# Optimization experiments

Measured on AMD Instinct MI355X. Metric: run time of the kernel, lower is better.

The kernel has to match this reference:

```python
import jax, jax.numpy as jnp
import numpy as np

TARGET_MAIN_CONTRIBUTION = 0.6
CONTRIB_LOSS_COEF = 0.01
TOP_K = 2
NEG_INF = -1e9


def _gat(x, adj, W1, a1s, a1d, W2, a2s, a2d):
    """Dense 2-layer GAT (pyGAT style): multi-head concat + ELU, then one output head.
    x: [B,S,Fin], adj: [B,S,S], W1: [H,Fin,Fh], a1s/a1d: [H,Fh], W2: [H*Fh,Fout], a2s/a2d: [Fout]."""
    mask = adj > 0  # [B,S,S]
    h = jnp.einsum('bsf,hfo->bhso', x, W1)                      # [B,H,S,Fh]
    es = jnp.einsum('bhso,ho->bhs', h, a1s)
    ed = jnp.einsum('bhso,ho->bhs', h, a1d)
    e = jax.nn.leaky_relu(es[:, :, :, None] + ed[:, :, None, :], 0.2)  # [B,H,S,S]
    att = jax.nn.softmax(jnp.where(mask[:, None], e, NEG_INF), axis=-1)
    h1 = jax.nn.elu(jnp.einsum('bhst,bhto->bhso', att, h))      # [B,H,S,Fh]
    B, H, S, Fh = h1.shape
    h1 = h1.transpose(0, 2, 1, 3).reshape(B, S, H * Fh)         # concat heads
    h2 = h1 @ W2                                                # [B,S,Fout]
    e2 = jax.nn.leaky_relu((h2 @ a2s)[:, :, None] + (h2 @ a2d)[:, None, :], 0.2)
    att2 = jax.nn.softmax(jnp.where(mask, e2, NEG_INF), axis=-1)
    return jnp.einsum('bst,bto->bso', att2, h2)


def setup_inputs() -> dict:
    B, S, D, H, Hd, E = 4, 1024, 256, 6, 64, 3
    key = jax.random.key(0)
    ks = jax.random.split(key, 20)
    feature = jax.random.normal(ks[0], (B, S, D), dtype=jnp.float32)
    # sparse-ish binary adjacency with self-loops
    adj = (jax.random.uniform(ks[1], (B, S, S)) < 0.05).astype(jnp.float32)
    adj = jnp.maximum(adj, jnp.eye(S, dtype=jnp.float32)[None])
    p = lambda k, shape: jax.random.normal(k, shape, dtype=jnp.float32) * 0.1
    return {
        'feature': feature, 'adj': adj,
        'main_W1': p(ks[2], (H, D, Hd)), 'main_a1s': p(ks[3], (H, Hd)), 'main_a1d': p(ks[4], (H, Hd)),
        'main_W2': p(ks[5], (H * Hd, D)), 'main_a2s': p(ks[6], (D,)), 'main_a2d': p(ks[7], (D,)),
        'dep_W1': p(ks[8], (E, H, D, Hd)), 'dep_a1s': p(ks[9], (E, H, Hd)), 'dep_a1d': p(ks[10], (E, H, Hd)),
        'dep_W2': p(ks[11], (E, H * Hd, D)), 'dep_a2s': p(ks[12], (E, D)), 'dep_a2d': p(ks[13], (E, D)),
        'router_W': p(ks[14], (D, E)),
        'blend_W': p(ks[15], (D, D)), 'blend_b': jnp.zeros((D,), dtype=jnp.float32),
        'doc_num': 4, 'sect_num': 32,
    }


def reference(feature, adj, main_W1, main_a1s, main_a1d, main_W2, main_a2s, main_a2d,
              dep_W1, dep_a1s, dep_a1d, dep_W2, dep_a2s, dep_a2d,
              router_W, blend_W, blend_b, doc_num, sect_num):
    B, S, D = feature.shape
    E = router_W.shape[1]
    # main expert on full graph
    main_output = _gat(feature, adj, main_W1, main_a1s, main_a1d, main_W2, main_a2s, main_a2d)
    # per-expert adjacency views (zero out columns by node type)
    col = jnp.arange(S)
    sent_cols = (col < S - sect_num - doc_num).astype(adj.dtype)
    sect_cols = ((col >= S - sect_num - doc_num) & (col < S - doc_num)).astype(adj.dtype)
    doc_cols = (col >= S - doc_num).astype(adj.dtype)
    adj_stack = jnp.stack([adj * sent_cols, adj * sect_cols, adj * doc_cols])  # [E,B,S,S]
    # fixed top-k router
    x_flat = feature.reshape(-1, D)
    gate_probs = jax.nn.softmax(x_flat @ router_W, axis=-1)      # [B*S,E]
    _, top_idx = jax.lax.top_k(gate_probs, TOP_K)                # [B*S,k]
    routing_mask = jax.nn.one_hot(top_idx, E, dtype=feature.dtype).sum(axis=-2)  # [B*S,E] binary
    routing_mask = routing_mask.reshape(B, S, E)
    mask_e = routing_mask.transpose(2, 0, 1)[..., None]          # [E,B,S,1]
    # deputy experts: masked input, masked output, accumulate
    x_e = feature[None] * mask_e                                 # [E,B,S,D]
    dep_out = jax.vmap(_gat)(x_e, adj_stack, dep_W1, dep_a1s, dep_a1d, dep_W2, dep_a2s, dep_a2d)
    deputy_output = (dep_out * mask_e).sum(axis=0)               # [B,S,D]
    # blend gate
    blend_weight = jax.nn.sigmoid(feature @ blend_W + blend_b)
    final_output = blend_weight * main_output + (1.0 - blend_weight) * deputy_output
    main_contribution = blend_weight.mean()
    contribution_loss = jnp.abs(main_contribution - TARGET_MAIN_CONTRIBUTION) * CONTRIB_LOSS_COEF
    return final_output, contribution_loss, main_contribution
```

## Files before the change

### kernel.cpp

```cpp
#include <hip/hip_runtime.h>
#include <math.h>

#define B 4
#define S 1024
#define D 256
#define H 6
#define HD 64
#define NE 3
#define HHD 384
#define ROWS (B*S)
#define MAXN 128

typedef __attribute__((ext_vector_type(8))) short bf8_t;
typedef __attribute__((ext_vector_type(4))) float f32x4;

__device__ __forceinline__ float leaky(float x){ return x > 0.f ? x : 0.2f*x; }

__device__ __forceinline__ unsigned short f2bf(float f){
    union { float f; unsigned int u; } v; v.f = f;
    unsigned int u = v.u;
    return (unsigned short)((u + 0x7FFFu + ((u >> 16) & 1u)) >> 16);
}
__device__ __forceinline__ float bf2f(unsigned short h){
    union { unsigned int u; float f; } v; v.u = ((unsigned int)h) << 16;
    return v.f;
}
__device__ __forceinline__ float blo(unsigned int u){
    union { unsigned int u; float f; } v; v.u = u << 16; return v.f;
}
__device__ __forceinline__ float bhi(unsigned int u){
    union { unsigned int u; float f; } v; v.u = u & 0xffff0000u; return v.f;
}
__device__ __forceinline__ float i2f(int t){
    union { int i; float f; } v; v.i = t; return v.f;
}
__device__ __forceinline__ int f2i(float f){
    union { float f; int i; } v; v.f = f; return v.i;
}

#define PB_CONV   1024
#define PB_NBR    1024
#define PB_W1     1536
#define PB_W2     1536
#define PB_BW      256
#define PB_ZERO    177
#define PB_ROUTER 1024
#define PB_TOTAL  (PB_CONV + PB_NBR + PB_W1 + PB_W2 + PB_BW + PB_ZERO + PB_ROUTER)
#define NZERO     45088

__global__ __launch_bounds__(256) void prep_misc_kernel(
        const float* __restrict__ feature, const float* __restrict__ adj,
        const float* __restrict__ main_W1, const float* __restrict__ dep_W1,
        const float* __restrict__ main_W2, const float* __restrict__ dep_W2,
        const float* __restrict__ blend_W, const float* __restrict__ router_W,
        const int* __restrict__ doc_p, const int* __restrict__ sect_p,
        unsigned short* __restrict__ featbf, short* __restrict__ nbr,
        int4* __restrict__ nbc, unsigned short* __restrict__ w1nk,
        unsigned short* __restrict__ w2nk, unsigned short* __restrict__ bwt,
        float* __restrict__ zbase, float* __restrict__ rmask)
{
    int blk = blockIdx.x, tid = threadIdx.x;
    if (blk < PB_CONV){
        int idx = blk*256 + tid;
        float4 v = ((const float4*)feature)[idx];
        ushort4 o;
        o.x = f2bf(v.x); o.y = f2bf(v.y); o.z = f2bf(v.z); o.w = f2bf(v.w);
        ((ushort4*)featbf)[idx] = o;
        return;
    }
    blk -= PB_CONV;
    if (blk < PB_NBR){
        int wave = tid >> 6, lane = tid & 63;
        int row = blk*4 + wave;
        int b1 = S - *sect_p - *doc_p;
        int b2 = S - *doc_p;
        const float* ar = adj + (size_t)row*S + lane*16;
        float a[16];
        #pragma unroll
        for (int q = 0; q < 4; q++){
            float4 v = ((const float4*)ar)[q];
            a[q*4+0] = v.x; a[q*4+1] = v.y; a[q*4+2] = v.z; a[q*4+3] = v.w;
        }
        int t0 = lane*16;
        int k = 0, c1 = 0, c2 = 0;
        #pragma unroll
        for (int i = 0; i < 16; i++){
            if (a[i] > 0.f){
                k++;
                int t = t0 + i;
                if (t < b1) c1++;
                if (t < b2) c2++;
            }
        }
        int inc = k;
        #pragma unroll
        for (int d = 1; d < 64; d <<= 1){
            int u = __shfl_up(inc, d);
            if (lane >= d) inc += u;
        }
        int off = inc - k;
        int total = __shfl(inc, 63);
        int o = row*MAXN + off;
        #pragma unroll
        for (int i = 0; i < 16; i++){
            if (a[i] > 0.f) nbr[o++] = (short)(t0 + i);
        }
        for (int d = 32; d; d >>= 1){
            c1 += __shfl_down(c1, d);
            c2 += __shfl_down(c2, d);
        }
        if (lane == 0) nbc[row] = make_int4(total, c1, c2, 0);
        return;
    }
    blk -= PB_NBR;
    if (blk < PB_W1){
        int e = blk / 384;
        int idx = (blk - e*384)*256 + tid;
        const float* src = (e == 0) ? main_W1 : dep_W1 + (size_t)(e-1)*H*D*HD;
        int n = idx >> 8, k = idx & 255;
        int h = n >> 6, o = n & 63;
        w1nk[(size_t)e*HHD*D + idx] = f2bf(src[(h*D + k)*HD + o]);
        return;
    }
    blk -= PB_W1;
    if (blk < PB_W2){
        int g = blk*256 + tid;
        int e = g / (D*HHD);
        int rem = g - e*(D*HHD);
        int n = rem / HHD, k = rem - n*HHD;
        const float* src = (e == 0) ? main_W2 : dep_W2 + (size_t)(e-1)*HHD*D;
        w2nk[g] = f2bf(src[k*D + n]);
        return;
    }
    blk -= PB_W2;
    if (blk < PB_BW){
        int col = blk, k = tid;
        bwt[col*D + k] = f2bf(blend_W[k*D + col]);
        return;
    }
    blk -= PB_BW;
    if (blk < PB_ZERO){
        int idx = blk*256 + tid;
        if (idx < NZERO) zbase[idx] = 0.f;
        return;
    }
    blk -= PB_ZERO;
    {
        int wave = tid >> 6, lane = tid & 63;
        int row = blk*4 + wave;
        float4 xv = ((const float4*)(feature + (size_t)row*D))[lane];
        int f = lane*4;
        float xa[4] = {xv.x, xv.y, xv.z, xv.w};
        float p0 = 0.f, p1 = 0.f, p2 = 0.f;
        #pragma unroll
        for (int j = 0; j < 4; j++){
            p0 += xa[j]*router_W[(f+j)*NE + 0];
            p1 += xa[j]*router_W[(f+j)*NE + 1];
            p2 += xa[j]*router_W[(f+j)*NE + 2];
        }
        for (int off = 32; off; off >>= 1){
            p0 += __shfl_down(p0, off);
            p1 += __shfl_down(p1, off);
            p2 += __shfl_down(p2, off);
        }
        if (lane == 0){
            float p[3] = {p0, p1, p2};
            int ex = 0;
            for (int e = 1; e < NE; e++) if (p[e] <= p[ex]) ex = e;
            for (int e = 0; e < NE; e++) rmask[e*ROWS + row] = (e == ex) ? 0.f : 1.f;
        }
    }
}

__global__ __launch_bounds__(256, 4) void gemm1_kernel(const unsigned short* __restrict__ w1nk,
                                                    const unsigned short* __restrict__ featbf,
                                                    const float* __restrict__ rmask,
                                                    const float* __restrict__ main_a1s,
                                                    const float* __restrict__ main_a1d,
                                                    const float* __restrict__ dep_a1s,
                                                    const float* __restrict__ dep_a1d,
                                                    const unsigned short* __restrict__ bwt,
                                                    const float* __restrict__ bb,
                                                    unsigned short* __restrict__ htn4,
                                                    float* __restrict__ es8,
                                                    float* __restrict__ ed8,
                                                    float* __restrict__ meanV1p,
                                                    float* __restrict__ gatebuf,
                                                    float* __restrict__ sumBuf){
    __shared__ float ep[2][2][64][17];
    int tid = threadIdx.x, wave = tid >> 6, lane = tid & 63;
    int quad = lane >> 4, l16 = lane & 15;
    int e = blockIdx.z;
    int n0 = blockIdx.y*64;
    f32x4 z4 = {0.f,0.f,0.f,0.f};
    bf8_t bz = {0,0,0,0,0,0,0,0};

    if (e == 4){
        if (blockIdx.x >= 2) return;
        int m0 = blockIdx.x*128;
        const unsigned short* arow0 = bwt + (size_t)(m0 + wave*16 + l16)*D + quad*8;
        const unsigned short* arow1 = arow0 + (size_t)64*D;
        const unsigned short* brow[4];
        #pragma unroll
        for (int j = 0; j < 4; j++)
            brow[j] = featbf + (size_t)(n0 + j*16 + l16)*D + quad*8;
        f32x4 acc[8] = {z4, z4, z4, z4, z4, z4, z4, z4};
        bf8_t a0F = *(const bf8_t*)(arow0);
        bf8_t a1F = *(const bf8_t*)(arow1);
        bf8_t bF[4];
        #pragma unroll
        for (int j = 0; j < 4; j++) bF[j] = *(const bf8_t*)(brow[j]);
        #pragma unroll
        for (int it = 0; it < D/32; it++){
            bf8_t a0C = a0F, a1C = a1F;
            bf8_t bC[4] = {bF[0], bF[1], bF[2], bF[3]};
            if (it + 1 < D/32){
                int kn = (it + 1)*32;
                a0F = *(const bf8_t*)(arow0 + kn);
                a1F = *(const bf8_t*)(arow1 + kn);
                #pragma unroll
                for (int j = 0; j < 4; j++) bF[j] = *(const bf8_t*)(brow[j] + kn);
            }
            #pragma unroll
            for (int j = 0; j < 4; j++){
                acc[j]   = __builtin_amdgcn_mfma_f32_16x16x32_bf16(a0C, bC[j], acc[j],   0, 0, 0);
                acc[4+j] = __builtin_amdgcn_mfma_f32_16x16x32_bf16(a1C, bC[j], acc[4+j], 0, 0, 0);
            }
        }
        int mbase0 = m0 + wave*16 + quad*4;
        int mbase1 = mbase0 + 64;
        float bias0[4], bias1[4];
        #pragma unroll
        for (int r = 0; r < 4; r++){ bias0[r] = bb[mbase0 + r]; bias1[r] = bb[mbase1 + r]; }
        float lsum = 0.f;
        #pragma unroll
        for (int j = 0; j < 4; j++){
            int rown = n0 + j*16 + l16;
            f32x4 st0, st1;
            #pragma unroll
            for (int r = 0; r < 4; r++){
                float g0 = 1.f/(1.f + __expf(-(acc[j][r] + bias0[r])));
                float g1 = 1.f/(1.f + __expf(-(acc[4+j][r] + bias1[r])));
                lsum += g0 + g1;
                st0[r] = g0; st1[r] = g1;
            }
            *(f32x4*)(gatebuf + (size_t)rown*D + mbase0) = st0;
            *(f32x4*)(gatebuf + (size_t)rown*D + mbase1) = st1;
        }
        float* redp = &ep[0][0][0][0];
        redp[tid] = lsum;
        __syncthreads();
        for (int sft = 128; sft; sft >>= 1){
            if (tid < sft) redp[tid] += redp[tid + sft];
            __syncthreads();
        }
        if (tid == 0) atomicAdd(sumBuf, redp[0]);
        return;
    }

    int p = blockIdx.x;
    int m0 = p*128;
    const unsigned short* arow0 = w1nk + (size_t)e*HHD*D + (size_t)(m0 + wave*16 + l16)*D + quad*8;
    const unsigned short* arow1 = arow0 + (size_t)64*D;
    const unsigned short* brow[4];
    bool zr[4];
    #pragma unroll
    for (int j = 0; j < 4; j++){
        int n = n0 + j*16 + l16;
        brow[j] = featbf + (size_t)n*D + quad*8;
        zr[j] = (e > 0) ? (rmask[(size_t)(e-1)*ROWS + n] == 0.f) : false;
    }
    f32x4 acc[8] = {z4, z4, z4, z4, z4, z4, z4, z4};
    bf8_t a0F = *(const bf8_t*)(arow0);
    bf8_t a1F = *(const bf8_t*)(arow1);
    bf8_t bF[4];
    #pragma unroll
    for (int j = 0; j < 4; j++) bF[j] = zr[j] ? bz : *(const bf8_t*)(brow[j]);
    #pragma unroll
    for (int it = 0; it < D/32; it++){
        bf8_t a0C = a0F, a1C = a1F;
        bf8_t bC[4] = {bF[0], bF[1], bF[2], bF[3]};
        if (it + 1 < D/32){
            int kn = (it + 1)*32;
            a0F = *(const bf8_t*)(arow0 + kn);
            a1F = *(const bf8_t*)(arow1 + kn);
            #pragma unroll
            for (int j = 0; j < 4; j++) bF[j] = zr[j] ? bz : *(const bf8_t*)(brow[j] + kn);
        }
        #pragma unroll
        for (int j = 0; j < 4; j++){
            acc[j]   = __builtin_amdgcn_mfma_f32_16x16x32_bf16(a0C, bC[j], acc[j],   0, 0, 0);
            acc[4+j] = __builtin_amdgcn_mfma_f32_16x16x32_bf16(a1C, bC[j], acc[4+j], 0, 0, 0);
        }
    }
    int b = n0 >> 10;
    int mbase0 = m0 + wave*16 + quad*4;
    int mbase1 = mbase0 + 64;
    int obase = wave*16 + quad*4;
    int h0 = p*2, h1 = p*2 + 1;
    #pragma unroll
    for (int j = 0; j < 4; j++){
        int row = n0 + j*16 + l16;
        ushort4 o0, o1;
        o0.x = f2bf(acc[j][0]);   o0.y = f2bf(acc[j][1]);
        o0.z = f2bf(acc[j][2]);   o0.w = f2bf(acc[j][3]);
        o1.x = f2bf(acc[4+j][0]); o1.y = f2bf(acc[4+j][1]);
        o1.z = f2bf(acc[4+j][2]); o1.w = f2bf(acc[4+j][3]);
        *(ushort4*)(htn4 + ((size_t)e*ROWS + row)*HHD + mbase0) = o0;
        *(ushort4*)(htn4 + ((size_t)e*ROWS + row)*HHD + mbase1) = o1;
    }
    const float* a1sp = (e == 0) ? main_a1s : dep_a1s + (size_t)(e-1)*H*HD;
    const float* a1dp = (e == 0) ? main_a1d : dep_a1d + (size_t)(e-1)*H*HD;
    float s0v[4], d0v[4], s1v[4], d1v[4];
    #pragma unroll
    for (int r = 0; r < 4; r++){
        s0v[r] = a1sp[mbase0 + r]; d0v[r] = a1dp[mbase0 + r];
        s1v[r] = a1sp[mbase1 + r]; d1v[r] = a1dp[mbase1 + r];
    }
    #pragma unroll
    for (int j = 0; j < 4; j++){
        float ps0 = 0.f, pd0 = 0.f, ps1 = 0.f, pd1 = 0.f;
        #pragma unroll
        for (int r = 0; r < 4; r++){
            ps0 += acc[j][r]*s0v[r];   pd0 += acc[j][r]*d0v[r];
            ps1 += acc[4+j][r]*s1v[r]; pd1 += acc[4+j][r]*d1v[r];
        }
        ep[0][0][j*16 + l16][wave*4 + quad] = ps0;
        ep[0][1][j*16 + l16][wave*4 + quad] = pd0;
        ep[1][0][j*16 + l16][wave*4 + quad] = ps1;
        ep[1][1][j*16 + l16][wave*4 + quad] = pd1;
    }
    float* mvb = meanV1p + ((size_t)e*B + b)*512;
    #pragma unroll
    for (int r = 0; r < 4; r++){
        float cm0 = acc[0][r] + acc[1][r] + acc[2][r] + acc[3][r];
        float cm1 = acc[4][r] + acc[5][r] + acc[6][r] + acc[7][r];
        for (int off = 8; off; off >>= 1){
            cm0 += __shfl_down(cm0, off, 16);
            cm1 += __shfl_down(cm1, off, 16);
        }
        if (l16 == 0){
            atomicAdd(mvb + (obase + r)*8 + h0, cm0*(1.f/(float)S));
            atomicAdd(mvb + (obase + r)*8 + h1, cm1*(1.f/(float)S));
        }
    }
    __syncthreads();
    {
        int hh = tid >> 7, arr = (tid >> 6) & 1, sl = tid & 63;
        float sum = 0.f;
        #pragma unroll
        for (int i = 0; i < 16; i++) sum += ep[hh][arr][sl][i];
        int n = n0 + sl;
        float* dst = arr ? ed8 : es8;
        dst[(((size_t)e*B + (n >> 10))*S + (n & 1023))*8 + (p*2 + hh)] = sum;
    }
}

__global__ __launch_bounds__(256) void attn1_gather_kernel(const unsigned short* __restrict__ htn4,
                                                           const float* __restrict__ es8,
                                                           const float* __restrict__ ed8,
                                                           const short* __restrict__ nbr,
                                                           const int4* __restrict__ nbc,
                                                           const float* __restrict__ meanV1p,
                                                           unsigned short* __restrict__ h1c4){
    __shared__ float wrec[4][MAXN][8];
    int wave = threadIdx.x >> 6, lane = threadIdx.x & 63;
    int s = blockIdx.x*4 + wave;
    int e = blockIdx.y >> 2, b = blockIdx.y & 3;
    int row = b*S + s;
    int4 c = nbc[row];
    int lo = 0, hi = c.x;
    if (e == 1) hi = c.y;
    else if (e == 2){ lo = c.y; hi = c.z; }
    else if (e == 3){ lo = c.z; }
    int nn = hi - lo;
    const float* esp = es8 + (((size_t)e*B + b)*S + s)*8;
    f32x4 es_lo = *(const f32x4*)esp;
    f32x4 es_hi = *(const f32x4*)(esp + 4);
    float esv[6] = {es_lo[0], es_lo[1], es_lo[2], es_lo[3], es_hi[0], es_hi[1]};
    const float* edb = ed8 + (((size_t)e*B + b)*S)*8;
    const short* nl = nbr + (size_t)row*MAXN;
    float w0[6] = {0,0,0,0,0,0}, w1[6] = {0,0,0,0,0,0};
    int t0 = 0, t1 = 0;
    if (lane < nn){
        t0 = nl[lo + lane];
        const float* ep = edb + (size_t)t0*8;
        f32x4 d0 = *(const f32x4*)ep;
        f32x4 d1 = *(const f32x4*)(ep + 4);
        float edv[6] = {d0[0], d0[1], d0[2], d0[3], d1[0], d1[1]};
        #pragma unroll
        for (int h = 0; h < 6; h++) w0[h] = __expf(leaky(esv[h] + edv[h]));
    }
    if (64 + lane < nn){
        t1 = nl[lo + 64 + lane];
        const float* ep = edb + (size_t)t1*8;
        f32x4 d0 = *(const f32x4*)ep;
        f32x4 d1 = *(const f32x4*)(ep + 4);
        float edv[6] = {d0[0], d0[1], d0[2], d0[3], d1[0], d1[1]};
        #pragma unroll
        for (int h = 0; h < 6; h++) w1[h] = __expf(leaky(esv[h] + edv[h]));
    }
    float den[6];
    #pragma unroll
    for (int h = 0; h < 6; h++){
        float d = w0[h] + w1[h];
        for (int o2 = 32; o2; o2 >>= 1) d += __shfl_down(d, o2);
        den[h] = __shfl(d, 0);
    }
    if (lane < nn){
        f32x4 r0 = {w0[0], w0[1], w0[2], w0[3]};
        f32x4 r1 = {w0[4], w0[5], i2f(t0), 0.f};
        *(f32x4*)&wrec[wave][lane][0] = r0;
        *(f32x4*)&wrec[wave][lane][4] = r1;
    }
    if (64 + lane < nn){
        f32x4 r0 = {w1[0], w1[1], w1[2], w1[3]};
        f32x4 r1 = {w1[4], w1[5], i2f(t1), 0.f};
        *(f32x4*)&wrec[wave][64 + lane][0] = r0;
        *(f32x4*)&wrec[wave][64 + lane][4] = r1;
    }
    const unsigned short* Vb = htn4 + ((size_t)e*ROWS + b*S)*HHD + lane;
    float acc[6] = {0,0,0,0,0,0};
    #pragma unroll 4
    for (int j = 0; j < nn; j++){
        f32x4 r0 = *(const f32x4*)&wrec[wave][j][0];
        f32x4 r1 = *(const f32x4*)&wrec[wave][j][4];
        int t = f2i(r1[2]);
        const unsigned short* vp = Vb + (size_t)t*HHD;
        float v0 = bf2f(vp[0]);
        float v1 = bf2f(vp[64]);
        float v2 = bf2f(vp[128]);
        float v3 = bf2f(vp[192]);
        float v4 = bf2f(vp[256]);
        float v5 = bf2f(vp[320]);
        acc[0] += r0[0]*v0; acc[1] += r0[1]*v1;
        acc[2] += r0[2]*v2; acc[3] += r0[3]*v3;
        acc[4] += r1[0]*v4; acc[5] += r1[1]*v5;
    }
    unsigned short* outp = h1c4 + ((size_t)e*ROWS + row)*HHD;
    const float* mv = meanV1p + ((size_t)e*B + b)*512 + lane*8;
    #pragma unroll
    for (int h = 0; h < 6; h++){
        float v = (nn > 0) ? acc[h]/den[h] : mv[h];
        v = v > 0.f ? v : __expf(v) - 1.f;
        outp[h*64 + lane] = f2bf(v);
    }
}

__global__ __launch_bounds__(256, 4) void gemm2_kernel(const unsigned short* __restrict__ w2nk,
                                                    const unsigned short* __restrict__ h1c4,
                                                    const float* __restrict__ main_a2s,
                                                    const float* __restrict__ main_a2d,
                                                    const float* __restrict__ dep_a2s,
                                                    const float* __restrict__ dep_a2d,
                                                    unsigned short* __restrict__ h2n4,
                                                    float* __restrict__ f2s4,
                                                    float* __restrict__ f2d4,
                                                    float* __restrict__ meanV2){
    __shared__ float ep[2][2][64][17];
    int tid = threadIdx.x, wave = tid >> 6, lane = tid & 63;
    int quad = lane >> 4, l16 = lane & 15;
    int e = blockIdx.z;
    int m0 = blockIdx.x*128;
    int n0 = blockIdx.y*64;
    f32x4 z4 = {0.f,0.f,0.f,0.f};
    const unsigned short* arow0 = w2nk + (size_t)e*D*HHD + (size_t)(m0 + wave*16 + l16)*HHD + quad*8;
    const unsigned short* arow1 = arow0 + (size_t)64*HHD;
    const unsigned short* brow[4];
    #pragma unroll
    for (int j = 0; j < 4; j++)
        brow[j] = h1c4 + (size_t)e*ROWS*HHD + (size_t)(n0 + j*16 + l16)*HHD + quad*8;
    f32x4 acc[8] = {z4, z4, z4, z4, z4, z4, z4, z4};
    bf8_t a0F = *(const bf8_t*)(arow0);
    bf8_t a1F = *(const bf8_t*)(arow1);
    bf8_t bF[4];
    #pragma unroll
    for (int j = 0; j < 4; j++) bF[j] = *(const bf8_t*)(brow[j]);
    #pragma unroll
    for (int it = 0; it < HHD/32; it++){
        bf8_t a0C = a0F, a1C = a1F;
        bf8_t bC[4] = {bF[0], bF[1], bF[2], bF[3]};
        if (it + 1 < HHD/32){
            int kn = (it + 1)*32;
            a0F = *(const bf8_t*)(arow0 + kn);
            a1F = *(const bf8_t*)(arow1 + kn);
            #pragma unroll
            for (int j = 0; j < 4; j++) bF[j] = *(const bf8_t*)(brow[j] + kn);
        }
        #pragma unroll
        for (int j = 0; j < 4; j++){
            acc[j]   = __builtin_amdgcn_mfma_f32_16x16x32_bf16(a0C, bC[j], acc[j],   0, 0, 0);
            acc[4+j] = __builtin_amdgcn_mfma_f32_16x16x32_bf16(a1C, bC[j], acc[4+j], 0, 0, 0);
        }
    }
    int b = n0 >> 10;
    int mbase0 = m0 + wave*16 + quad*4;
    int mbase1 = mbase0 + 64;
    #pragma unroll
    for (int j = 0; j < 4; j++){
        int row = n0 + j*16 + l16;
        ushort4 o0, o1;
        o0.x = f2bf(acc[j][0]);   o0.y = f2bf(acc[j][1]);
        o0.z = f2bf(acc[j][2]);   o0.w = f2bf(acc[j][3]);
        o1.x = f2bf(acc[4+j][0]); o1.y = f2bf(acc[4+j][1]);
        o1.z = f2bf(acc[4+j][2]); o1.w = f2bf(acc[4+j][3]);
        *(ushort4*)(h2n4 + ((size_t)e*ROWS + row)*D + mbase0) = o0;
        *(ushort4*)(h2n4 + ((size_t)e*ROWS + row)*D + mbase1) = o1;
    }
    const float* a2sp = (e == 0) ? main_a2s : dep_a2s + (size_t)(e-1)*D;
    const float* a2dp = (e == 0) ? main_a2d : dep_a2d + (size_t)(e-1)*D;
    float s0v[4], d0v[4], s1v[4], d1v[4];
    #pragma unroll
    for (int r = 0; r < 4; r++){
        s0v[r] = a2sp[mbase0 + r]; d0v[r] = a2dp[mbase0 + r];
        s1v[r] = a2sp[mbase1 + r]; d1v[r] = a2dp[mbase1 + r];
    }
    #pragma unroll
    for (int j = 0; j < 4; j++){
        float ps0 = 0.f, pd0 = 0.f, ps1 = 0.f, pd1 = 0.f;
        #pragma unroll
        for (int r = 0; r < 4; r++){
            ps0 += acc[j][r]*s0v[r];   pd0 += acc[j][r]*d0v[r];
            ps1 += acc[4+j][r]*s1v[r]; pd1 += acc[4+j][r]*d1v[r];
        }
        ep[0][0][j*16 + l16][wave*4 + quad] = ps0;
        ep[0][1][j*16 + l16][wave*4 + quad] = pd0;
        ep[1][0][j*16 + l16][wave*4 + quad] = ps1;
        ep[1][1][j*16 + l16][wave*4 + quad] = pd1;
    }
    #pragma unroll
    for (int r = 0; r < 4; r++){
        float cm0 = acc[0][r] + acc[1][r] + acc[2][r] + acc[3][r];
        float cm1 = acc[4][r] + acc[5][r] + acc[6][r] + acc[7][r];
        for (int off = 8; off; off >>= 1){
            cm0 += __shfl_down(cm0, off, 16);
            cm1 += __shfl_down(cm1, off, 16);
        }
        if (l16 == 0){
            atomicAdd(meanV2 + ((size_t)e*B + b)*D + mbase0 + r, cm0*(1.f/(float)S));
            atomicAdd(meanV2 + ((size_t)e*B + b)*D + mbase1 + r, cm1*(1.f/(float)S));
        }
    }
    __syncthreads();
    {
        int hh = tid >> 7, arr = (tid >> 6) & 1, sl = tid & 63;
        float sum = 0.f;
        #pragma unroll
        for (int i = 0; i < 16; i++) sum += ep[hh][arr][sl][i];
        int n = n0 + sl;
        float* dst = arr ? f2d4 : f2s4;
        atomicAdd(dst + (size_t)e*ROWS + n, sum);
    }
}

__global__ __launch_bounds__(256) void attn2_blend_kernel(const unsigned short* __restrict__ h2n4,
                                                          const float* __restrict__ f2s4,
                                                          const float* __restrict__ f2d4,
                                                          const short* __restrict__ nbr,
                                                          const int4* __restrict__ nbc,
                                                          const float* __restrict__ meanV2,
                                                          const float* __restrict__ gatebuf,
                                                          const float* __restrict__ rmask,
                                                          const float* __restrict__ sumBuf,
                                                          float* __restrict__ outp){
    __shared__ float2 wrec[4][MAXN];
    __shared__ float outs[4][256];
    int wave = threadIdx.x >> 6, lane = threadIdx.x & 63;
    int s = blockIdx.x, b = blockIdx.y;
    int e = wave;
    int row = b*S + s;
    int4 c = nbc[row];
    int lo = 0, hi = c.x;
    if (e == 1) hi = c.y;
    else if (e == 2){ lo = c.y; hi = c.z; }
    else if (e == 3){ lo = c.z; }
    int nn = hi - lo;
    float fs_r = f2s4[(size_t)e*ROWS + row];
    const float* fdp = f2d4 + (size_t)e*ROWS + b*S;
    const short* nl = nbr + (size_t)row*MAXN;
    float w0 = 0.f, w1 = 0.f;
    int t0 = 0, t1 = 0;
    if (lane < nn){ t0 = nl[lo + lane]; w0 = __expf(leaky(fs_r + fdp[t0])); }
    if (64 + lane < nn){ t1 = nl[lo + 64 + lane]; w1 = __expf(leaky(fs_r + fdp[t1])); }
    float den = w0 + w1;
    for (int o2 = 32; o2; o2 >>= 1) den += __shfl_down(den, o2);
    den = __shfl(den, 0);
    if (lane < nn){ float2 r; r.x = w0; r.y = i2f(t0); wrec[wave][lane] = r; }
    if (64 + lane < nn){ float2 r; r.x = w1; r.y = i2f(t1); wrec[wave][64 + lane] = r; }
    const unsigned short* V = h2n4 + ((size_t)e*ROWS + b*S)*D;
    float acc[4] = {0,0,0,0};
    #pragma unroll 4
    for (int j = 0; j < nn; j++){
        float2 r = wrec[wave][j];
        float w = r.x;
        int t = f2i(r.y);
        const unsigned short* vp = V + (size_t)t*D + lane*4;
        uint2 dv = *(const uint2*)vp;
        acc[0] += w*blo(dv.x); acc[1] += w*bhi(dv.x);
        acc[2] += w*blo(dv.y); acc[3] += w*bhi(dv.y);
    }
    if (nn > 0){
        float inv = 1.f/den;
        #pragma unroll
        for (int q = 0; q < 4; q++) outs[e][lane*4 + q] = acc[q]*inv;
    } else {
        const float* mv = meanV2 + ((size_t)e*B + b)*D + lane*4;
        #pragma unroll
        for (int q = 0; q < 4; q++) outs[e][lane*4 + q] = mv[q];
    }
    __syncthreads();
    int col = threadIdx.x;
    float g = gatebuf[(size_t)row*D + col];
    float rm0 = rmask[row], rm1 = rmask[ROWS + row], rm2 = rmask[2*ROWS + row];
    float dep = rm0*outs[1][col] + rm1*outs[2][col] + rm2*outs[3][col];
    outp[(size_t)row*D + col] = g*outs[0][col] + (1.f - g)*dep;
    if (blockIdx.x == 0 && blockIdx.y == 0 && threadIdx.x == 0){
        float mc = sumBuf[0] / (float)(ROWS*D);
        outp[ROWS*D]     = fabsf(mc - 0.6f)*0.01f;
        outp[ROWS*D + 1] = mc;
    }
}

extern "C" void kernel_launch(void* const* d_in, const int* in_sizes, int n_in,
                              void* d_out, int out_size, void* d_ws, size_t ws_size,
                              hipStream_t stream)
{
    const float* feature  = (const float*)d_in[0];
    const float* adj      = (const float*)d_in[1];
    const float* main_W1  = (const float*)d_in[2];
    const float* main_a1s = (const float*)d_in[3];
    const float* main_a1d = (const float*)d_in[4];
    const float* main_W2  = (const float*)d_in[5];
    const float* main_a2s = (const float*)d_in[6];
    const float* main_a2d = (const float*)d_in[7];
    const float* dep_W1   = (const float*)d_in[8];
    const float* dep_a1s  = (const float*)d_in[9];
    const float* dep_a1d  = (const float*)d_in[10];
    const float* dep_W2   = (const float*)d_in[11];
    const float* dep_a2s  = (const float*)d_in[12];
    const float* dep_a2d  = (const float*)d_in[13];
    const float* router_W = (const float*)d_in[14];
    const float* blend_W  = (const float*)d_in[15];
    const float* blend_b  = (const float*)d_in[16];
    const int*   doc_p    = (const int*)d_in[17];
    const int*   sect_p   = (const int*)d_in[18];

    char* ws = (char*)d_ws;
    size_t off = 0;
    unsigned short* featbf = (unsigned short*)(ws + off); off += (size_t)ROWS*D*2;
    short*          nbr    = (short*)(ws + off);          off += (size_t)ROWS*MAXN*2;
    int4*           nbc    = (int4*)(ws + off);           off += (size_t)ROWS*16;
    unsigned short* w1nk   = (unsigned short*)(ws + off); off += (size_t)4*HHD*D*2;
    unsigned short* w2nk   = (unsigned short*)(ws + off); off += (size_t)4*D*HHD*2;
    unsigned short* bwt    = (unsigned short*)(ws + off); off += (size_t)D*D*2;
    float* es8 = (float*)(ws + off); off += (size_t)4*B*S*8*4;
    float* ed8 = (float*)(ws + off); off += (size_t)4*B*S*8*4;
    float* gatebuf = (float*)(ws + off); off += (size_t)ROWS*D*4;
    unsigned short* htn4 = (unsigned short*)(ws + off); off += (size_t)4*ROWS*HHD*2;
    unsigned short* h2n4 = (unsigned short*)(ws + off); off += (size_t)4*ROWS*D*2;
    unsigned short* h1c4 = (unsigned short*)(ws + off); off += (size_t)4*ROWS*HHD*2;
    float* f2s4    = (float*)(ws + off); off += (size_t)4*ROWS*4;
    float* f2d4    = (float*)(ws + off); off += (size_t)4*ROWS*4;
    float* meanV1p = (float*)(ws + off); off += (size_t)4*B*512*4;
    float* meanV2  = (float*)(ws + off); off += (size_t)4*B*D*4;
    float* sumBuf  = (float*)(ws + off); off += 128;
    float* rmask   = (float*)(ws + off); off += (size_t)NE*ROWS*4;
    float* outp    = (float*)d_out;

    prep_misc_kernel<<<PB_TOTAL, 256, 0, stream>>>(
        feature, adj, main_W1, dep_W1, main_W2, dep_W2, blend_W, router_W,
        doc_p, sect_p, featbf, nbr, nbc, w1nk, w2nk, bwt, f2s4, rmask);

    gemm1_kernel<<<dim3(3, ROWS/64, 5), 256, 0, stream>>>(w1nk, featbf, rmask,
        main_a1s, main_a1d, dep_a1s, dep_a1d, bwt, blend_b,
        htn4, es8, ed8, meanV1p, gatebuf, sumBuf);
    attn1_gather_kernel<<<dim3(S/4, 16), 256, 0, stream>>>(htn4, es8, ed8, nbr, nbc,
        meanV1p, h1c4);
    gemm2_kernel<<<dim3(D/128, ROWS/64, 4), 256, 0, stream>>>(w2nk, h1c4,
        main_a2s, main_a2d, dep_a2s, dep_a2d, h2n4, f2s4, f2d4, meanV2);
    attn2_blend_kernel<<<dim3(S, B), 256, 0, stream>>>(h2n4, f2s4, f2d4, nbr, nbc,
        meanV2, gatebuf, rmask, sumBuf, outp);
}
```

Measured before the change: 210.5 us.

## Split neighbor gathers across waves and skip inactive experts in attention layer 2

The layer-1 gather now gives each row two waves that split the neighbor list and combine partial sums and denominators through shared memory. This is meant to balance per-row work and raise parallelism. The layer-2 blend kernel now uses two waves for the main expert and two for the deputy experts, and it skips deputy experts the router did not select, since their outputs are masked to zero anyway. This adds more barriers and shared-memory reduction traffic, and it changes the per-wave load pattern.

```diff
diff --git a/kernel.cpp b/kernel.cpp
--- a/kernel.cpp
+++ b/kernel.cpp
@@ -356,16 +356,18 @@
     }
 }
 
-__global__ __launch_bounds__(256) void attn1_gather_kernel(const unsigned short* __restrict__ htn4,
+__global__ __launch_bounds__(128) void attn1_gather_kernel(const unsigned short* __restrict__ htn4,
                                                            const float* __restrict__ es8,
                                                            const float* __restrict__ ed8,
                                                            const short* __restrict__ nbr,
                                                            const int4* __restrict__ nbc,
                                                            const float* __restrict__ meanV1p,
                                                            unsigned short* __restrict__ h1c4){
-    __shared__ float wrec[4][MAXN][8];
+    __shared__ float wrec[MAXN][8];
+    __shared__ float pacc[64][8];
+    __shared__ float pden[2][8];
     int wave = threadIdx.x >> 6, lane = threadIdx.x & 63;
-    int s = blockIdx.x*4 + wave;
+    int s = blockIdx.x;
     int e = blockIdx.y >> 2, b = blockIdx.y & 3;
     int row = b*S + s;
     int4 c = nbc[row];
@@ -378,53 +380,36 @@
     f32x4 es_lo = *(const f32x4*)esp;
     f32x4 es_hi = *(const f32x4*)(esp + 4);
     float esv[6] = {es_lo[0], es_lo[1], es_lo[2], es_lo[3], es_hi[0], es_hi[1]};
-    const float* edb = ed8 + (((size_t)e*B + b)*S)*8;
+    const float* edb = ed8 + ((size_t)e*B + b)*S*8;
     const short* nl = nbr + (size_t)row*MAXN;
-    float w0[6] = {0,0,0,0,0,0}, w1[6] = {0,0,0,0,0,0};
-    int t0 = 0, t1 = 0;
-    if (lane < nn){
-        t0 = nl[lo + lane];
-        const float* ep = edb + (size_t)t0*8;
-        f32x4 d0 = *(const f32x4*)ep;
-        f32x4 d1 = *(const f32x4*)(ep + 4);
+    int i = wave*64 + lane;
+    float w[6] = {0,0,0,0,0,0};
+    if (i < nn){
+        int t = nl[lo + i];
+        const float* epn = edb + (size_t)t*8;
+        f32x4 d0 = *(const f32x4*)epn;
+        f32x4 d1 = *(const f32x4*)(epn + 4);
         float edv[6] = {d0[0], d0[1], d0[2], d0[3], d1[0], d1[1]};
         #pragma unroll
-        for (int h = 0; h < 6; h++) w0[h] = __expf(leaky(esv[h] + edv[h]));
-    }
-    if (64 + lane < nn){
-        t1 = nl[lo + 64 + lane];
-        const float* ep = edb + (size_t)t1*8;
-        f32x4 d0 = *(const f32x4*)ep;
-        f32x4 d1 = *(const f32x4*)(ep + 4);
-        float edv[6] = {d0[0], d0[1], d0[2], d0[3], d1[0], d1[1]};
-        #pragma unroll
-        for (int h = 0; h < 6; h++) w1[h] = __expf(leaky(esv[h] + edv[h]));
-    }
-    float den[6];
+        for (int h = 0; h < 6; h++) w[h] = __expf(leaky(esv[h] + edv[h]));
+        f32x4 r0 = {w[0], w[1], w[2], w[3]};
+        f32x4 r1 = {w[4], w[5], i2f(t), 0.f};
+        *(f32x4*)&wrec[i][0] = r0;
+        *(f32x4*)&wrec[i][4] = r1;
+    }
     #pragma unroll
     for (int h = 0; h < 6; h++){
-        float d = w0[h] + w1[h];
-        for (int o2 = 32; o2; o2 >>= 1) d += __shfl_down(d, o2);
-        den[h] = __shfl(d, 0);
-    }
-    if (lane < nn){
-        f32x4 r0 = {w0[0], w0[1], w0[2], w0[3]};
-        f32x4 r1 = {w0[4], w0[5], i2f(t0), 0.f};
-        *(f32x4*)&wrec[wave][lane][0] = r0;
-        *(f32x4*)&wrec[wave][lane][4] = r1;
-    }
-    if (64 + lane < nn){
-        f32x4 r0 = {w1[0], w1[1], w1[2], w1[3]};
-        f32x4 r1 = {w1[4], w1[5], i2f(t1), 0.f};
-        *(f32x4*)&wrec[wave][64 + lane][0] = r0;
-        *(f32x4*)&wrec[wave][64 + lane][4] = r1;
-    }
+        float x = w[h];
+        for (int o2 = 32; o2; o2 >>= 1) x += __shfl_down(x, o2);
+        if (lane == 0) pden[wave][h] = x;
+    }
+    __syncthreads();
     const unsigned short* Vb = htn4 + ((size_t)e*ROWS + b*S)*HHD + lane;
     float acc[6] = {0,0,0,0,0,0};
     #pragma unroll 4
-    for (int j = 0; j < nn; j++){
-        f32x4 r0 = *(const f32x4*)&wrec[wave][j][0];
-        f32x4 r1 = *(const f32x4*)&wrec[wave][j][4];
+    for (int j = wave; j < nn; j += 2){
+        f32x4 r0 = *(const f32x4*)&wrec[j][0];
+        f32x4 r1 = *(const f32x4*)&wrec[j][4];
         int t = f2i(r1[2]);
         const unsigned short* vp = Vb + (size_t)t*HHD;
         float v0 = bf2f(vp[0]);
@@ -437,13 +422,23 @@
         acc[2] += r0[2]*v2; acc[3] += r0[3]*v3;
         acc[4] += r1[0]*v4; acc[5] += r1[1]*v5;
     }
-    unsigned short* outp = h1c4 + ((size_t)e*ROWS + row)*HHD;
-    const float* mv = meanV1p + ((size_t)e*B + b)*512 + lane*8;
-    #pragma unroll
-    for (int h = 0; h < 6; h++){
-        float v = (nn > 0) ? acc[h]/den[h] : mv[h];
-        v = v > 0.f ? v : __expf(v) - 1.f;
-        outp[h*64 + lane] = f2bf(v);
+    if (wave == 1){
+        f32x4 p0 = {acc[0], acc[1], acc[2], acc[3]};
+        f32x4 p1 = {acc[4], acc[5], 0.f, 0.f};
+        *(f32x4*)&pacc[lane][0] = p0;
+        *(f32x4*)&pacc[lane][4] = p1;
+    }
+    __syncthreads();
+    if (wave == 0){
+        unsigned short* outp = h1c4 + ((size_t)e*ROWS + row)*HHD;
+        const float* mv = meanV1p + ((size_t)e*B + b)*512 + lane*8;
+        #pragma unroll
+        for (int h = 0; h < 6; h++){
+            float den = pden[0][h] + pden[1][h];
+            float v = (nn > 0) ? (acc[h] + pacc[lane][h])/den : mv[h];
+            v = v > 0.f ? v : __expf(v) - 1.f;
+            outp[h*64 + lane] = f2bf(v);
+        }
     }
 }
 
@@ -563,57 +558,118 @@
                                                           const float* __restrict__ rmask,
                                                           const float* __restrict__ sumBuf,
                                                           float* __restrict__ outp){
-    __shared__ float2 wrec[4][MAXN];
-    __shared__ float outs[4][256];
+    __shared__ float2 wrec0[MAXN];
+    __shared__ float2 wrec1[MAXN];
+    __shared__ float pacc[3][256];
+    __shared__ float pden[4][4];
     int wave = threadIdx.x >> 6, lane = threadIdx.x & 63;
     int s = blockIdx.x, b = blockIdx.y;
-    int e = wave;
     int row = b*S + s;
     int4 c = nbc[row];
-    int lo = 0, hi = c.x;
-    if (e == 1) hi = c.y;
-    else if (e == 2){ lo = c.y; hi = c.z; }
-    else if (e == 3){ lo = c.z; }
-    int nn = hi - lo;
-    float fs_r = f2s4[(size_t)e*ROWS + row];
-    const float* fdp = f2d4 + (size_t)e*ROWS + b*S;
+    float rm0 = rmask[row], rm1 = rmask[ROWS + row], rm2 = rmask[2*ROWS + row];
     const short* nl = nbr + (size_t)row*MAXN;
-    float w0 = 0.f, w1 = 0.f;
-    int t0 = 0, t1 = 0;
-    if (lane < nn){ t0 = nl[lo + lane]; w0 = __expf(leaky(fs_r + fdp[t0])); }
-    if (64 + lane < nn){ t1 = nl[lo + 64 + lane]; w1 = __expf(leaky(fs_r + fdp[t1])); }
-    float den = w0 + w1;
-    for (int o2 = 32; o2; o2 >>= 1) den += __shfl_down(den, o2);
-    den = __shfl(den, 0);
-    if (lane < nn){ float2 r; r.x = w0; r.y = i2f(t0); wrec[wave][lane] = r; }
-    if (64 + lane < nn){ float2 r; r.x = w1; r.y = i2f(t1); wrec[wave][64 + lane] = r; }
-    const unsigned short* V = h2n4 + ((size_t)e*ROWS + b*S)*D;
-    float acc[4] = {0,0,0,0};
-    #pragma unroll 4
-    for (int j = 0; j < nn; j++){
-        float2 r = wrec[wave][j];
-        float w = r.x;
-        int t = f2i(r.y);
-        const unsigned short* vp = V + (size_t)t*D + lane*4;
-        uint2 dv = *(const uint2*)vp;
-        acc[0] += w*blo(dv.x); acc[1] += w*bhi(dv.x);
-        acc[2] += w*blo(dv.y); acc[3] += w*bhi(dv.y);
-    }
-    if (nn > 0){
-        float inv = 1.f/den;
-        #pragma unroll
-        for (int q = 0; q < 4; q++) outs[e][lane*4 + q] = acc[q]*inv;
+    if (wave < 2){
+        int i = wave*64 + lane;
+        float w = 0.f;
+        if (i < c.x){
+            int t = nl[i];
+            float fs = f2s4[row];
+            w = __expf(leaky(fs + f2d4[(size_t)b*S + t]));
+            float2 r; r.x = w; r.y = i2f(t);
+            wrec0[i] = r;
+        }
+        float dsum = w;
+        for (int o2 = 32; o2; o2 >>= 1) dsum += __shfl_down(dsum, o2);
+        if (lane == 0) pden[wave][0] = dsum;
     } else {
-        const float* mv = meanV2 + ((size_t)e*B + b)*D + lane*4;
-        #pragma unroll
-        for (int q = 0; q < 4; q++) outs[e][lane*4 + q] = mv[q];
+        int i = (wave - 2)*64 + lane;
+        float w = 0.f, d1 = 0.f, d2 = 0.f, d3 = 0.f;
+        if (i < c.x){
+            int t = nl[i];
+            int tag = (i < c.y) ? 1 : ((i < c.z) ? 2 : 3);
+            float act = (tag == 1) ? rm0 : ((tag == 2) ? rm1 : rm2);
+            if (act != 0.f){
+                float fs = f2s4[(size_t)tag*ROWS + row];
+                w = __expf(leaky(fs + f2d4[(size_t)tag*ROWS + (size_t)b*S + t]));
+            }
+            float2 r; r.x = w; r.y = i2f(t);
+            wrec1[i] = r;
+            if (tag == 1) d1 = w; else if (tag == 2) d2 = w; else d3 = w;
+        }
+        for (int o2 = 32; o2; o2 >>= 1){
+            d1 += __shfl_down(d1, o2);
+            d2 += __shfl_down(d2, o2);
+            d3 += __shfl_down(d3, o2);
+        }
+        if (lane == 0){ pden[wave][1] = d1; pden[wave][2] = d2; pden[wave][3] = d3; }
     }
     __syncthreads();
-    int col = threadIdx.x;
-    float g = gatebuf[(size_t)row*D + col];
-    float rm0 = rmask[row], rm1 = rmask[ROWS + row], rm2 = rmask[2*ROWS + row];
-    float dep = rm0*outs[1][col] + rm1*outs[2][col] + rm2*outs[3][col];
-    outp[(size_t)row*D + col] = g*outs[0][col] + (1.f - g)*dep;
+    float acc[4] = {0.f, 0.f, 0.f, 0.f};
+    if (wave < 2){
+        float inv = 1.f/(pden[0][0] + pden[1][0]);
+        const unsigned short* V = h2n4 + (size_t)b*S*D;
+        #pragma unroll 4
+        for (int j = wave; j < c.x; j += 2){
+            float2 r = wrec0[j];
+            float wv = r.x*inv;
+            int t = f2i(r.y);
+            const unsigned short* vp = V + (size_t)t*D + lane*4;
+            uint2 dv = *(const uint2*)vp;
+            acc[0] += wv*blo(dv.x); acc[1] += wv*bhi(dv.x);
+            acc[2] += wv*blo(dv.y); acc[3] += wv*bhi(dv.y);
+        }
+    } else {
+        int rlo[3] = {0, c.y, c.z};
+        int rhi[3] = {c.y, c.z, c.x};
+        float ract[3] = {rm0, rm1, rm2};
+        for (int rg = 0; rg < 3; rg++){
+            if (ract[rg] == 0.f || rhi[rg] <= rlo[rg]) continue;
+            float inv = 1.f/(pden[2][rg+1] + pden[3][rg+1]);
+            const unsigned short* V = h2n4 + ((size_t)(rg+1)*ROWS + (size_t)b*S)*D;
+            #pragma unroll 4
+            for (int j = rlo[rg] + (wave - 2); j < rhi[rg]; j += 2){
+                float2 r = wrec1[j];
+                float wv = r.x*inv;
+                int t = f2i(r.y);
+                const unsigned short* vp = V + (size_t)t*D + lane*4;
+                uint2 dv = *(const uint2*)vp;
+                acc[0] += wv*blo(dv.x); acc[1] += wv*bhi(dv.x);
+                acc[2] += wv*blo(dv.y); acc[3] += wv*bhi(dv.y);
+            }
+        }
+    }
+    if (wave >= 1){
+        #pragma unroll
+        for (int q = 0; q < 4; q++) pacc[wave-1][lane*4 + q] = acc[q];
+    }
+    __syncthreads();
+    if (wave == 0){
+        float4 g4 = *(const float4*)(gatebuf + (size_t)row*D + lane*4);
+        float dep_mv[4] = {0.f, 0.f, 0.f, 0.f};
+        if (rm0 != 0.f && c.y == 0){
+            float4 mv = *(const float4*)(meanV2 + ((size_t)1*B + b)*D + lane*4);
+            dep_mv[0] += mv.x; dep_mv[1] += mv.y; dep_mv[2] += mv.z; dep_mv[3] += mv.w;
+        }
+        if (rm1 != 0.f && c.z == c.y){
+            float4 mv = *(const float4*)(meanV2 + ((size_t)2*B + b)*D + lane*4);
+            dep_mv[0] += mv.x; dep_mv[1] += mv.y; dep_mv[2] += mv.z; dep_mv[3] += mv.w;
+        }
+        if (rm2 != 0.f && c.x == c.z){
+            float4 mv = *(const float4*)(meanV2 + ((size_t)3*B + b)*D + lane*4);
+            dep_mv[0] += mv.x; dep_mv[1] += mv.y; dep_mv[2] += mv.z; dep_mv[3] += mv.w;
+        }
+        float g[4] = {g4.x, g4.y, g4.z, g4.w};
+        float4 o;
+        float* op = &o.x;
+        #pragma unroll
+        for (int q = 0; q < 4; q++){
+            int col = lane*4 + q;
+            float a0 = acc[q] + pacc[0][col];
+            float dep = pacc[1][col] + pacc[2][col] + dep_mv[q];
+            op[q] = g[q]*a0 + (1.f - g[q])*dep;
+        }
+        *(float4*)(outp + (size_t)row*D + lane*4) = o;
+    }
     if (blockIdx.x == 0 && blockIdx.y == 0 && threadIdx.x == 0){
         float mc = sumBuf[0] / (float)(ROWS*D);
         outp[ROWS*D]     = fabsf(mc - 0.6f)*0.01f;
@@ -674,7 +730,7 @@
     gemm1_kernel<<<dim3(3, ROWS/64, 5), 256, 0, stream>>>(w1nk, featbf, rmask,
         main_a1s, main_a1d, dep_a1s, dep_a1d, bwt, blend_b,
         htn4, es8, ed8, meanV1p, gatebuf, sumBuf);
-    attn1_gather_kernel<<<dim3(S/4, 16), 256, 0, stream>>>(htn4, es8, ed8, nbr, nbc,
+    attn1_gather_kernel<<<dim3(S, 16), 128, 0, stream>>>(htn4, es8, ed8, nbr, nbc,
         meanV1p, h1c4);
     gemm2_kernel<<<dim3(D/128, ROWS/64, 4), 256, 0, stream>>>(w2nk, h1c4,
         main_a2s, main_a2d, dep_a2s, dep_a2d, h2n4, f2s4, f2d4, meanV2);
```

Result: no change. 212.3 us (+0.8%).
